# Performance work log

Hardware: AMD Instinct MI355X
Metric: run time of the kernel (lower is better)

The kernel has to match this reference:

```python
import jax, jax.numpy as jnp
import numpy as np
import math

NUM_HEADS = 16

def setup_inputs() -> dict:
    key = jax.random.key(0)
    k1, k2, k3 = jax.random.split(key, 3)
    B, L, C = 4, 2048, 1024
    # xavier-uniform-ish scale for weights
    input = jax.random.normal(k1, (B, L, C), dtype=jnp.float32)
    w_in = jax.random.uniform(k2, (3 * C, C), dtype=jnp.float32, minval=-1.0, maxval=1.0) * math.sqrt(6.0 / (4 * C))
    w_out = jax.random.uniform(k3, (C, C), dtype=jnp.float32, minval=-1.0, maxval=1.0) * math.sqrt(6.0 / (2 * C))
    return {"input": input, "w_in": w_in, "w_out": w_out}

def reference(input, w_in, w_out):
    B, L, C = input.shape
    H = NUM_HEADS
    D = C // H
    qkv = input @ w_in.T                      # [B, L, 3C]
    q, k, v = jnp.split(qkv, 3, axis=-1)
    # [B, H, L, D]
    q = q.reshape(B, L, H, D).transpose(0, 2, 1, 3)
    k = k.reshape(B, L, H, D).transpose(0, 2, 1, 3)
    v = v.reshape(B, L, H, D).transpose(0, 2, 1, 3)
    scale = 1.0 / math.sqrt(D)
    scores = scale * jnp.einsum('bhqd,bhkd->bhqk', q, k)  # [B, H, L, L]
    causal = jnp.tril(jnp.ones((L, L), dtype=bool))
    scores = jnp.where(causal, scores, -jnp.inf)
    attn = jax.nn.softmax(scores, axis=-1)
    ctx = jnp.einsum('bhqk,bhkd->bhqd', attn, v)          # [B, H, L, D]
    ctx = ctx.transpose(0, 2, 1, 3).reshape(B, L, C)
    return ctx @ w_out.T
```

## Files before the change

kernel.cpp:

```cpp
#include <hip/hip_runtime.h>
#include <math.h>

typedef __bf16 bf16_t;
typedef __attribute__((ext_vector_type(8))) __bf16 bf16x8;
typedef __attribute__((ext_vector_type(4))) float f32x4;
typedef __attribute__((ext_vector_type(16))) float f32x16;

#define AS_G __attribute__((address_space(1)))
#define AS_L __attribute__((address_space(3)))

__device__ __forceinline__ f32x4 mfma16(bf16x8 a, bf16x8 b, f32x4 c) {
  return __builtin_amdgcn_mfma_f32_16x16x32_bf16(a, b, c, 0, 0, 0);
}
__device__ __forceinline__ f32x16 mfma32(bf16x8 a, bf16x8 b, f32x16 c) {
  return __builtin_amdgcn_mfma_f32_32x32x16_bf16(a, b, c, 0, 0, 0);
}

__device__ __forceinline__ void gload16(const bf16_t* g, bf16_t* l) {
  __builtin_amdgcn_global_load_lds((const AS_G void*)g, (AS_L void*)l, 16, 0, 0);
}

__global__ void cvt_f32_bf16_k(const float* __restrict__ in, bf16_t* __restrict__ out, int n4) {
  int i = blockIdx.x * blockDim.x + threadIdx.x;
  int stride = gridDim.x * blockDim.x;
  for (; i < n4; i += stride) {
    float4 v = reinterpret_cast<const float4*>(in)[i];
    union { bf16_t b[4]; short4 s; } u;
    u.b[0] = (bf16_t)v.x; u.b[1] = (bf16_t)v.y;
    u.b[2] = (bf16_t)v.z; u.b[3] = (bf16_t)v.w;
    reinterpret_cast<short4*>(out)[i] = u.s;
  }
}

template <int EPI>
__global__ __launch_bounds__(256)
void gemm_bt(const bf16_t* __restrict__ A, const bf16_t* __restrict__ Bm,
             bf16_t* __restrict__ q_out, bf16_t* __restrict__ k_out,
             bf16_t* __restrict__ vt_out, float* __restrict__ f_out,
             int M, int N, int K) {
  __shared__ __align__(16) bf16_t lA[128 * 32];
  __shared__ __align__(16) bf16_t lB[128 * 32];
  const int lane = threadIdx.x & 63;
  const int wid = threadIdx.x >> 6;
  const int m0 = blockIdx.y * 128;
  const int n0 = blockIdx.x * 128;
  const int wr = (wid >> 1) * 64;
  const int wc = (wid & 1) * 64;
  const int lr = lane & 15;
  const int lg = lane >> 4;
  const int srow = lane >> 2;
  const int scol = (lane & 3) * 8;
  const int s0 = wid * 2, s1 = s0 + 1;

  f32x4 acc[4][4] = {};

  for (int k0 = 0; k0 < K; k0 += 32) {
    gload16(A + (size_t)(m0 + s0 * 16 + srow) * K + k0 + scol, &lA[s0 * 512]);
    gload16(A + (size_t)(m0 + s1 * 16 + srow) * K + k0 + scol, &lA[s1 * 512]);
    gload16(Bm + (size_t)(n0 + s0 * 16 + srow) * K + k0 + scol, &lB[s0 * 512]);
    gload16(Bm + (size_t)(n0 + s1 * 16 + srow) * K + k0 + scol, &lB[s1 * 512]);
    __syncthreads();
    bf16x8 af[4], bfr[4];
#pragma unroll
    for (int m = 0; m < 4; ++m)
      af[m] = *reinterpret_cast<const bf16x8*>(&lA[(wr + m * 16 + lr) * 32 + lg * 8]);
#pragma unroll
    for (int n = 0; n < 4; ++n)
      bfr[n] = *reinterpret_cast<const bf16x8*>(&lB[(wc + n * 16 + lr) * 32 + lg * 8]);
#pragma unroll
    for (int m = 0; m < 4; ++m)
#pragma unroll
      for (int n = 0; n < 4; ++n)
        acc[m][n] = mfma16(af[m], bfr[n], acc[m][n]);
    __syncthreads();
  }

  if (EPI == 0) {
#pragma unroll
    for (int n = 0; n < 4; ++n) {
      const int gn = n0 + wc + n * 16 + lr;
      const int sec = gn >> 10;
      const int hd = gn & 1023;
      const int h = hd >> 6, d = hd & 63;
#pragma unroll
      for (int m = 0; m < 4; ++m) {
        const int gm0 = m0 + wr + m * 16 + lg * 4;
        if (sec == 0) {
#pragma unroll
          for (int r = 0; r < 4; ++r) {
            const int gm = gm0 + r;
            q_out[((size_t)((gm >> 11) * 16 + h) * 2048 + (gm & 2047)) * 64 + d] =
                (bf16_t)(acc[m][n][r] * 0.125f);
          }
        } else if (sec == 1) {
#pragma unroll
          for (int r = 0; r < 4; ++r) {
            const int gm = gm0 + r;
            k_out[((size_t)((gm >> 11) * 16 + h) * 2048 + (gm & 2047)) * 64 + d] =
                (bf16_t)acc[m][n][r];
          }
        } else {
          union { bf16_t b[4]; short4 s; } u;
#pragma unroll
          for (int r = 0; r < 4; ++r) u.b[r] = (bf16_t)acc[m][n][r];
          const int b = gm0 >> 11, sl = gm0 & 2047;
          *reinterpret_cast<short4*>(
              &vt_out[((size_t)(b * 16 + h) * 64 + d) * 2048 + sl]) = u.s;
        }
      }
    }
  } else {
#pragma unroll
    for (int m = 0; m < 4; ++m) {
      const int gm0 = m0 + wr + m * 16 + lg * 4;
#pragma unroll
      for (int n = 0; n < 4; ++n) {
        const int gn = n0 + wc + n * 16 + lr;
#pragma unroll
        for (int r = 0; r < 4; ++r)
          f_out[(size_t)(gm0 + r) * N + gn] = acc[m][n][r];
      }
    }
  }
}

__device__ __forceinline__ void attn_tile(
    const bf16_t* __restrict__ tK, const bf16_t* __restrict__ tV,
    int kb, int q0w, int qrow, int q32, int hi,
    const bf16x8 bq[4], f32x16 oacc[2], float& m_run, float& l_run) {
  f32x16 sacc[2] = {};
#pragma unroll
  for (int n = 0; n < 2; ++n) {
    const int row = n * 32 + q32;
    const int rx = row & 7;
#pragma unroll
    for (int c = 0; c < 4; ++c) {
      bf16x8 ak = *reinterpret_cast<const bf16x8*>(
          &tK[row * 64 + ((2 * c + hi) ^ rx) * 8]);
      sacc[n] = mfma32(ak, bq[c], sacc[n]);
    }
  }
  if (kb + 63 > q0w) {
#pragma unroll
    for (int n = 0; n < 2; ++n)
#pragma unroll
      for (int r = 0; r < 16; ++r) {
        const int kg = kb + n * 32 + (r & 3) + 4 * hi + 8 * (r >> 2);
        if (kg > qrow) sacc[n][r] = -1e30f;
      }
  }
  float v8[8];
#pragma unroll
  for (int i = 0; i < 8; ++i)
    v8[i] = fmaxf(fmaxf(sacc[0][i], sacc[0][i + 8]),
                  fmaxf(sacc[1][i], sacc[1][i + 8]));
  float pm = fmaxf(fmaxf(fmaxf(v8[0], v8[4]), fmaxf(v8[1], v8[5])),
                   fmaxf(fmaxf(v8[2], v8[6]), fmaxf(v8[3], v8[7])));
  pm = fmaxf(pm, __shfl_xor(pm, 32));
  if (__any(pm > m_run + 8.f)) {
    const float mn = fmaxf(m_run, pm);
    const float al = __expf(m_run - mn);
#pragma unroll
    for (int ms = 0; ms < 2; ++ms)
#pragma unroll
      for (int r = 0; r < 16; ++r) oacc[ms][r] *= al;
    l_run *= al;
    m_run = mn;
  }
  float ls = 0.f;
#pragma unroll
  for (int n = 0; n < 2; ++n)
#pragma unroll
    for (int r = 0; r < 16; ++r) {
      const float p = __expf(sacc[n][r] - m_run);
      sacc[n][r] = p;
      ls += p;
    }
  ls += __shfl_xor(ls, 32);
  l_run += ls;
  bf16x8 pb[4];
#pragma unroll
  for (int n = 0; n < 2; ++n) {
    int w[8], pw[8];
#pragma unroll
    for (int j = 0; j < 8; ++j) {
      union { bf16_t b[2]; int i; } u;
      u.b[0] = (bf16_t)sacc[n][2 * j];
      u.b[1] = (bf16_t)sacc[n][2 * j + 1];
      w[j] = u.i;
    }
#pragma unroll
    for (int j = 0; j < 8; ++j) pw[j] = __shfl_xor(w[j], 32);
#pragma unroll
    for (int s = 0; s < 2; ++s) {
      union { int i[4]; bf16x8 v; } pv;
      if (hi == 0) {
        pv.i[0] = w[4 * s];      pv.i[1] = w[4 * s + 1];
        pv.i[2] = pw[4 * s];     pv.i[3] = pw[4 * s + 1];
      } else {
        pv.i[0] = pw[4 * s + 2]; pv.i[1] = pw[4 * s + 3];
        pv.i[2] = w[4 * s + 2];  pv.i[3] = w[4 * s + 3];
      }
      pb[2 * n + s] = pv.v;
    }
  }
#pragma unroll
  for (int s4 = 0; s4 < 4; ++s4) {
#pragma unroll
    for (int ms = 0; ms < 2; ++ms) {
      const int row = ms * 32 + q32;
      bf16x8 av = *reinterpret_cast<const bf16x8*>(
          &tV[row * 64 + ((2 * s4 + hi) ^ (row & 7)) * 8]);
      oacc[ms] = mfma32(av, pb[s4], oacc[ms]);
    }
  }
}

__device__ __forceinline__ void attn_epi(bf16_t* __restrict__ ctx, int bh,
                                         int qrow, int hi,
                                         const f32x16 oacc[2], float l_run) {
  const float inv = 1.f / l_run;
  const int b = bh >> 4, h = bh & 15;
  const size_t orow = (size_t)(b * 2048 + qrow) * 1024 + h * 64;
#pragma unroll
  for (int ms = 0; ms < 2; ++ms)
#pragma unroll
    for (int rg = 0; rg < 4; ++rg) {
      union { bf16_t b4[4]; short4 s; } u;
#pragma unroll
      for (int i = 0; i < 4; ++i) u.b4[i] = (bf16_t)(oacc[ms][rg * 4 + i] * inv);
      *reinterpret_cast<short4*>(&ctx[orow + ms * 32 + rg * 8 + hi * 4]) = u.s;
    }
}

__global__ __launch_bounds__(256)
void attn_fwd(const bf16_t* __restrict__ Q, const bf16_t* __restrict__ Km,
              const bf16_t* __restrict__ Vt, bf16_t* __restrict__ ctx, int L) {
  __shared__ __align__(16) bf16_t lK[2][64 * 64];
  __shared__ __align__(16) bf16_t lV[2][64 * 64];

  const int lane = threadIdx.x & 63;
  const int wid = threadIdx.x >> 6;
  const int nid = (blockIdx.x & 7) * 64 + (blockIdx.x >> 3);
  const int bh = nid >> 3;
  const int p = nid & 7;
  const int jA = 15 - p, jB = p;
  const int q32 = lane & 31;
  const int hi = lane >> 5;
  const int q0A = jA * 128 + wid * 32, qrowA = q0A + q32;
  const int q0B = jB * 128 + wid * 32, qrowB = q0B + q32;
  const bf16_t* Qh = Q + (size_t)bh * L * 64;
  const bf16_t* Kh = Km + (size_t)bh * L * 64;
  const bf16_t* Vh = Vt + (size_t)bh * 64 * L;

  bf16x8 bqA[4], bqB[4];
#pragma unroll
  for (int c = 0; c < 4; ++c) {
    bqA[c] = *reinterpret_cast<const bf16x8*>(&Qh[(size_t)qrowA * 64 + c * 16 + hi * 8]);
    bqB[c] = *reinterpret_cast<const bf16x8*>(&Qh[(size_t)qrowB * 64 + c * 16 + hi * 8]);
  }

  f32x16 oaccA[2] = {}, oaccB[2] = {};
  float mA = -1e30f, lA_ = 0.f, mB = -1e30f, lB_ = 0.f;

  const int sr0 = wid * 8 + (lane >> 3);
  const int sc = ((lane & 7) ^ (sr0 & 7)) * 8;
  const int nt = 2 * jA + 2;

#define STAGE(buf, kb)                                                      \
  do {                                                                      \
    gload16(Kh + (size_t)((kb) + sr0) * 64 + sc, &lK[buf][wid * 512]);      \
    gload16(Kh + (size_t)((kb) + sr0 + 32) * 64 + sc,                       \
            &lK[buf][2048 + wid * 512]);                                    \
    gload16(Vh + (size_t)sr0 * L + (kb) + sc, &lV[buf][wid * 512]);         \
    gload16(Vh + (size_t)(sr0 + 32) * L + (kb) + sc,                        \
            &lV[buf][2048 + wid * 512]);                                    \
  } while (0)

  STAGE(0, 0);
  int cur = 0;
  for (int t = 0; t < nt; ++t) {
    __syncthreads();
    if (t + 1 < nt) STAGE(cur ^ 1, (t + 1) * 64);
    const int kb = t * 64;
    const bf16_t* tK = lK[cur];
    const bf16_t* tV = lV[cur];
    if (kb <= q0A + 31)
      attn_tile(tK, tV, kb, q0A, qrowA, q32, hi, bqA, oaccA, mA, lA_);
    if (kb <= q0B + 31)
      attn_tile(tK, tV, kb, q0B, qrowB, q32, hi, bqB, oaccB, mB, lB_);
    cur ^= 1;
  }
#undef STAGE
  attn_epi(ctx, bh, qrowA, hi, oaccA, lA_);
  attn_epi(ctx, bh, qrowB, hi, oaccB, lB_);
}

extern "C" void kernel_launch(void* const* d_in, const int* in_sizes, int n_in,
                              void* d_out, int out_size, void* d_ws, size_t ws_size,
                              hipStream_t stream) {
  (void)in_sizes; (void)n_in; (void)out_size; (void)ws_size;
  const float* x     = (const float*)d_in[0];
  const float* w_in  = (const float*)d_in[1];
  const float* w_out = (const float*)d_in[2];
  float* out = (float*)d_out;

  char* ws = (char*)d_ws;
  bf16_t* xb   = (bf16_t*)(ws);
  bf16_t* wib  = (bf16_t*)(ws + 16777216);
  bf16_t* wob  = (bf16_t*)(ws + 23068672);
  bf16_t* Qb   = (bf16_t*)(ws + 25165824);
  bf16_t* Kb   = (bf16_t*)(ws + 41943040);
  bf16_t* Vtb  = (bf16_t*)(ws + 58720256);
  bf16_t* ctxb = (bf16_t*)(ws + 75497472);

  const int M = 8192, C = 1024, L = 2048;

  {
    int n4 = 8388608 / 4, blk = (n4 + 255) / 256; if (blk > 2048) blk = 2048;
    cvt_f32_bf16_k<<<blk, 256, 0, stream>>>(x, xb, n4);
  }
  {
    int n4 = 3145728 / 4, blk = (n4 + 255) / 256; if (blk > 2048) blk = 2048;
    cvt_f32_bf16_k<<<blk, 256, 0, stream>>>(w_in, wib, n4);
  }
  {
    int n4 = 1048576 / 4, blk = (n4 + 255) / 256; if (blk > 2048) blk = 2048;
    cvt_f32_bf16_k<<<blk, 256, 0, stream>>>(w_out, wob, n4);
  }

  gemm_bt<0><<<dim3(3072 / 128, M / 128), 256, 0, stream>>>(
      xb, wib, Qb, Kb, Vtb, nullptr, M, 3072, C);

  attn_fwd<<<512, 256, 0, stream>>>(Qb, Kb, Vtb, ctxb, L);

  gemm_bt<1><<<dim3(C / 128, M / 128), 256, 0, stream>>>(
      ctxb, wob, nullptr, nullptr, nullptr, out, M, C, C);
}
```

Before: 282.4 us.

## Split attention query tiles across 8 waves and fold log2e into Q scale

The attention kernel now runs 512 threads per block. Two wave groups each own one of the paired causal query tiles instead of each wave processing both, and the K and V staging is split between the groups. The Q scale now includes log2(e), so the softmax can use exp2f instead of __expf. This is meant to raise wave-level parallelism and cut per-wave register pressure and serial work. The cost is that the group with the short tile sits idle at barriers while the long tile finishes.

```diff
diff --git a/kernel.cpp b/kernel.cpp
--- a/kernel.cpp
+++ b/kernel.cpp
@@ -90,7 +90,7 @@
           for (int r = 0; r < 4; ++r) {
             const int gm = gm0 + r;
             q_out[((size_t)((gm >> 11) * 16 + h) * 2048 + (gm & 2047)) * 64 + d] =
-                (bf16_t)(acc[m][n][r] * 0.125f);
+                (bf16_t)(acc[m][n][r] * 0.18033688f);
           }
         } else if (sec == 1) {
 #pragma unroll
@@ -159,7 +159,7 @@
   pm = fmaxf(pm, __shfl_xor(pm, 32));
   if (__any(pm > m_run + 8.f)) {
     const float mn = fmaxf(m_run, pm);
-    const float al = __expf(m_run - mn);
+    const float al = exp2f(m_run - mn);
 #pragma unroll
     for (int ms = 0; ms < 2; ++ms)
 #pragma unroll
@@ -172,7 +172,7 @@
   for (int n = 0; n < 2; ++n)
 #pragma unroll
     for (int r = 0; r < 16; ++r) {
-      const float p = __expf(sacc[n][r] - m_run);
+      const float p = exp2f(sacc[n][r] - m_run);
       sacc[n][r] = p;
       ls += p;
     }
@@ -233,7 +233,7 @@
     }
 }
 
-__global__ __launch_bounds__(256)
+__global__ __launch_bounds__(512, 4)
 void attn_fwd(const bf16_t* __restrict__ Q, const bf16_t* __restrict__ Km,
               const bf16_t* __restrict__ Vt, bf16_t* __restrict__ ctx, int L) {
   __shared__ __align__(16) bf16_t lK[2][64 * 64];
@@ -241,40 +241,44 @@
 
   const int lane = threadIdx.x & 63;
   const int wid = threadIdx.x >> 6;
+  const int w4 = wid & 3;
+  const int grp = wid >> 2;
   const int nid = (blockIdx.x & 7) * 64 + (blockIdx.x >> 3);
   const int bh = nid >> 3;
   const int p = nid & 7;
   const int jA = 15 - p, jB = p;
   const int q32 = lane & 31;
   const int hi = lane >> 5;
-  const int q0A = jA * 128 + wid * 32, qrowA = q0A + q32;
-  const int q0B = jB * 128 + wid * 32, qrowB = q0B + q32;
+  const int j = grp ? jB : jA;
+  const int q0 = j * 128 + w4 * 32;
+  const int qrow = q0 + q32;
   const bf16_t* Qh = Q + (size_t)bh * L * 64;
   const bf16_t* Kh = Km + (size_t)bh * L * 64;
   const bf16_t* Vh = Vt + (size_t)bh * 64 * L;
 
-  bf16x8 bqA[4], bqB[4];
-#pragma unroll
-  for (int c = 0; c < 4; ++c) {
-    bqA[c] = *reinterpret_cast<const bf16x8*>(&Qh[(size_t)qrowA * 64 + c * 16 + hi * 8]);
-    bqB[c] = *reinterpret_cast<const bf16x8*>(&Qh[(size_t)qrowB * 64 + c * 16 + hi * 8]);
-  }
-
-  f32x16 oaccA[2] = {}, oaccB[2] = {};
-  float mA = -1e30f, lA_ = 0.f, mB = -1e30f, lB_ = 0.f;
-
-  const int sr0 = wid * 8 + (lane >> 3);
+  bf16x8 bq[4];
+#pragma unroll
+  for (int c = 0; c < 4; ++c)
+    bq[c] = *reinterpret_cast<const bf16x8*>(&Qh[(size_t)qrow * 64 + c * 16 + hi * 8]);
+
+  f32x16 oacc[2] = {};
+  float m_run = -1e30f, l_run = 0.f;
+
+  const int sr0 = w4 * 8 + (lane >> 3);
   const int sc = ((lane & 7) ^ (sr0 & 7)) * 8;
   const int nt = 2 * jA + 2;
 
-#define STAGE(buf, kb)                                                      \
-  do {                                                                      \
-    gload16(Kh + (size_t)((kb) + sr0) * 64 + sc, &lK[buf][wid * 512]);      \
-    gload16(Kh + (size_t)((kb) + sr0 + 32) * 64 + sc,                       \
-            &lK[buf][2048 + wid * 512]);                                    \
-    gload16(Vh + (size_t)sr0 * L + (kb) + sc, &lV[buf][wid * 512]);         \
-    gload16(Vh + (size_t)(sr0 + 32) * L + (kb) + sc,                        \
-            &lV[buf][2048 + wid * 512]);                                    \
+#define STAGE(buf, kb)                                                        \
+  do {                                                                        \
+    if (grp == 0) {                                                           \
+      gload16(Kh + (size_t)((kb) + sr0) * 64 + sc, &lK[buf][w4 * 512]);       \
+      gload16(Kh + (size_t)((kb) + sr0 + 32) * 64 + sc,                       \
+              &lK[buf][2048 + w4 * 512]);                                     \
+    } else {                                                                  \
+      gload16(Vh + (size_t)sr0 * L + (kb) + sc, &lV[buf][w4 * 512]);          \
+      gload16(Vh + (size_t)(sr0 + 32) * L + (kb) + sc,                        \
+              &lV[buf][2048 + w4 * 512]);                                     \
+    }                                                                         \
   } while (0)
 
   STAGE(0, 0);
@@ -283,17 +287,12 @@
     __syncthreads();
     if (t + 1 < nt) STAGE(cur ^ 1, (t + 1) * 64);
     const int kb = t * 64;
-    const bf16_t* tK = lK[cur];
-    const bf16_t* tV = lV[cur];
-    if (kb <= q0A + 31)
-      attn_tile(tK, tV, kb, q0A, qrowA, q32, hi, bqA, oaccA, mA, lA_);
-    if (kb <= q0B + 31)
-      attn_tile(tK, tV, kb, q0B, qrowB, q32, hi, bqB, oaccB, mB, lB_);
+    if (kb <= q0 + 31)
+      attn_tile(lK[cur], lV[cur], kb, q0, qrow, q32, hi, bq, oacc, m_run, l_run);
     cur ^= 1;
   }
 #undef STAGE
-  attn_epi(ctx, bh, qrowA, hi, oaccA, lA_);
-  attn_epi(ctx, bh, qrowB, hi, oaccB, lB_);
+  attn_epi(ctx, bh, qrow, hi, oacc, l_run);
 }
 
 extern "C" void kernel_launch(void* const* d_in, const int* in_sizes, int n_in,
@@ -332,7 +331,7 @@
   gemm_bt<0><<<dim3(3072 / 128, M / 128), 256, 0, stream>>>(
       xb, wib, Qb, Kb, Vtb, nullptr, M, 3072, C);
 
-  attn_fwd<<<512, 256, 0, stream>>>(Qb, Kb, Vtb, ctxb, L);
+  attn_fwd<<<512, 512, 0, stream>>>(Qb, Kb, Vtb, ctxb, L);
 
   gemm_bt<1><<<dim3(C / 128, M / 128), 256, 0, stream>>>(
       ctxb, wob, nullptr, nullptr, nullptr, out, M, C, C);
```

New measurement: 285.1 us. About the same (+0.9%).
